# Kernel tuning notes

Measured on AMD Instinct MI355X. Metric: run time of the kernel, lower is better.

## Reference

```python
import jax, jax.numpy as jnp
import numpy as np
from jax import lax

WIN = 9
PAD = WIN // 2
DIM = 3
WIN_VOL = WIN ** DIM  # 729
EPS_DENOM = 1e-05


def _box_sum(x):
    # x: (N, 1, D, H, W); all-ones WINxWINxWIN box filter, 'same' padding
    kernel = jnp.ones((1, 1, WIN, WIN, WIN), dtype=x.dtype)
    return lax.conv_general_dilated(
        x, kernel,
        window_strides=(1, 1, 1),
        padding=[(PAD, PAD)] * 3,
        dimension_numbers=("NCDHW", "OIDHW", "NCDHW"),
    )


def setup_inputs() -> dict:
    key = jax.random.key(0)
    k1, k2 = jax.random.split(key)
    shape = (2, 1, 160, 192, 160)
    I = jax.random.uniform(k1, shape, dtype=jnp.float32)
    J = jax.random.uniform(k2, shape, dtype=jnp.float32)
    return {"I": I, "J": J}


def reference(I, J):
    n = I.shape[0]
    # Fuse the five box-filter convs into one by stacking along the batch dim
    stacked = jnp.concatenate([I, J, I * I, J * J, I * J], axis=0)
    sums = _box_sum(stacked)
    I_sum, J_sum, I2_sum, J2_sum, IJ_sum = (
        sums[0 * n:1 * n], sums[1 * n:2 * n], sums[2 * n:3 * n],
        sums[3 * n:4 * n], sums[4 * n:5 * n],
    )
    wv = jnp.asarray(WIN_VOL, dtype=I.dtype)
    E_I = I_sum / wv
    E_J = J_sum / wv
    cross = IJ_sum - I_sum * E_J - J_sum * E_I + E_I * E_J * wv
    I_var = I2_sum - 2 * E_I * I_sum + E_I * E_I * wv
    J_var = J2_sum - 2 * E_J * J_sum + E_J * E_J * wv
    cc = cross * cross / (I_var * J_var + EPS_DENOM)
    return -jnp.mean(cc)
```

## Files before the change

kernel.cpp:

```cpp
#include <hip/hip_runtime.h>


namespace {
constexpr int Wd = 160, Hd = 192, Dd = 160, NB = 2;
constexpr long DSTRIDE = (long)Hd * Wd;
constexpr long VOLUME  = (long)Dd * DSTRIDE;
constexpr long TOTAL   = VOLUME * NB;
constexpr int BW = 32, BH = 16, BD = 28;
constexpr int EH = BH + 8;
constexpr int NWB = 5, NHB = 12, NDB = 6;
constexpr int NBLK = NB * NDB * NHB * NWB;
constexpr int NT = 512;
constexpr int CH  = EH * BW;
constexpr int HWC = BH * BW;
constexpr float INV_WV = 1.0f / 729.0f;
}

__device__ __forceinline__ void bar_lds() {
    asm volatile("s_waitcnt lgkmcnt(0)\n\ts_barrier" ::: "memory");
}

__device__ __forceinline__ float4 slide9(float v0, float v1, float v2, float v3,
                                         float v4, float v5, float v6, float v7,
                                         float v8, float v9, float v10, float v11) {
    float s8 = ((v0 + v1) + (v2 + v3)) + ((v4 + v5) + (v6 + v7)) + v8;
    float4 o;
    o.x = s8;
    o.y = o.x + (v9 - v0);
    o.z = o.y + (v10 - v1);
    o.w = o.z + (v11 - v2);
    return o;
}

__global__ __launch_bounds__(NT) void k_ncc(const float* __restrict__ I,
                                            const float* __restrict__ J,
                                            float* __restrict__ partial) {
    __shared__ float ws[5 * CH];
    __shared__ float hw[5 * HWC];
    __shared__ float red[NT];

    const int tid = threadIdx.x;
    int bx = blockIdx.x;
    const int wb = bx % NWB; bx /= NWB;
    const int hb = bx % NHB; bx /= NHB;
    const int db = bx % NDB; bx /= NDB;
    const int n  = bx;
    const int w0 = wb * BW, h0 = hb * BH, d0 = db * BD;
    const long nvol = (long)n * VOLUME;

    const int seg = tid & 7;
    const int yy  = tid >> 3;
    const bool aJob = (tid < 192);
    const int ah    = h0 - 4 + yy;
    const int wbase = w0 - 4 + (seg << 2);
    const bool ahOk = aJob && ((unsigned)ah < (unsigned)Hd);
    const bool qok0 = ((unsigned)(wbase + 0) < (unsigned)Wd);
    const bool qok1 = ((unsigned)(wbase + 4) < (unsigned)Wd);
    const bool qok2 = ((unsigned)(wbase + 8) < (unsigned)Wd);
    const long roff = nvol + (long)ah * Wd + wbase + (long)(d0 - 4) * DSTRIDE;
    const float* aI = I + roff;
    const float* aJ = J + roff;

    const int c2  = tid >> 6;
    const int ho0 = ((tid >> 5) & 1) * 8;
    const int w2  = tid & 31;

    const int tx = tid & 31, ty = tid >> 5;

    float4 pI0, pI1, pI2, pJ0, pJ1, pJ2;

#define ISSUE(PP)                                                            \
    do {                                                                     \
        const bool _pv = ahOk && ((unsigned)(PP) < (unsigned)Dd);            \
        pI0 = (_pv && qok0) ? *(const float4*)(aI + 0) : float4{0, 0, 0, 0}; \
        pI1 = (_pv && qok1) ? *(const float4*)(aI + 4) : float4{0, 0, 0, 0}; \
        pI2 = (_pv && qok2) ? *(const float4*)(aI + 8) : float4{0, 0, 0, 0}; \
        pJ0 = (_pv && qok0) ? *(const float4*)(aJ + 0) : float4{0, 0, 0, 0}; \
        pJ1 = (_pv && qok1) ? *(const float4*)(aJ + 4) : float4{0, 0, 0, 0}; \
        pJ2 = (_pv && qok2) ? *(const float4*)(aJ + 8) : float4{0, 0, 0, 0}; \
    } while (0)

    float hist[9][5];
#pragma unroll
    for (int k = 0; k < 9; ++k)
#pragma unroll
        for (int c = 0; c < 5; ++c) hist[k][c] = 0.0f;
    float sa[5] = {0, 0, 0, 0, 0};
    float acc = 0.0f;

    ISSUE(d0 - 4);

#pragma unroll 1
    for (int M = 0; M < 4; ++M) {
#pragma unroll
        for (int u = 0; u < 9; ++u) {
            const int t = 9 * M + u;
            const int p = d0 - 4 + t;
            const bool pvalid = ((unsigned)p < (unsigned)Dd);

            if (pvalid && aJob) {
                const float a0 = pI0.x, a1 = pI0.y, a2 = pI0.z, a3 = pI0.w;
                const float a4 = pI1.x, a5 = pI1.y, a6 = pI1.z, a7 = pI1.w;
                const float a8 = pI2.x, a9 = pI2.y, a10 = pI2.z, a11 = pI2.w;
                const float b0 = pJ0.x, b1 = pJ0.y, b2 = pJ0.z, b3 = pJ0.w;
                const float b4 = pJ1.x, b5 = pJ1.y, b6 = pJ1.z, b7 = pJ1.w;
                const float b8 = pJ2.x, b9 = pJ2.y, b10 = pJ2.z, b11 = pJ2.w;
                float* const wab = ws + yy * BW + (seg << 2);
                *(float4*)(wab + 0 * CH) =
                    slide9(a0, a1, a2, a3, a4, a5, a6, a7, a8, a9, a10, a11);
                *(float4*)(wab + 1 * CH) =
                    slide9(b0, b1, b2, b3, b4, b5, b6, b7, b8, b9, b10, b11);
                *(float4*)(wab + 2 * CH) =
                    slide9(a0 * a0, a1 * a1, a2 * a2, a3 * a3, a4 * a4, a5 * a5,
                           a6 * a6, a7 * a7, a8 * a8, a9 * a9, a10 * a10, a11 * a11);
                *(float4*)(wab + 3 * CH) =
                    slide9(b0 * b0, b1 * b1, b2 * b2, b3 * b3, b4 * b4, b5 * b5,
                           b6 * b6, b7 * b7, b8 * b8, b9 * b9, b10 * b10, b11 * b11);
                *(float4*)(wab + 4 * CH) =
                    slide9(a0 * b0, a1 * b1, a2 * b2, a3 * b3, a4 * b4, a5 * b5,
                           a6 * b6, a7 * b7, a8 * b8, a9 * b9, a10 * b10, a11 * b11);
            }
            aI += DSTRIDE; aJ += DSTRIDE;
            ISSUE(p + 1);

            bar_lds();

            if (pvalid && tid < 320) {
                const float* const src = ws + c2 * CH + ho0 * BW + w2;
                float* const dst = hw + c2 * HWC + ho0 * BW + w2;
                float s = ((src[0 * BW] + src[1 * BW]) + (src[2 * BW] + src[3 * BW]))
                        + ((src[4 * BW] + src[5 * BW]) + (src[6 * BW] + src[7 * BW]));
#pragma unroll
                for (int k = 0; k < 8; ++k) {
                    s += src[(k + 8) * BW];
                    dst[k * BW] = s;
                    s -= src[k * BW];
                }
            }

            bar_lds();

            float h5[5];
            if (pvalid) {
#pragma unroll
                for (int c = 0; c < 5; ++c)
                    h5[c] = hw[c * HWC + ty * BW + tx];
            } else {
#pragma unroll
                for (int c = 0; c < 5; ++c) h5[c] = 0.0f;
            }
#pragma unroll
            for (int c = 0; c < 5; ++c) sa[c] += h5[c];
            const int dout = d0 + t - 8;
            if (t >= 8 && dout < Dd) {
                const float cross = sa[4] - sa[0] * sa[1] * INV_WV;
                const float iv    = sa[2] - sa[0] * sa[0] * INV_WV;
                const float jv    = sa[3] - sa[1] * sa[1] * INV_WV;
                acc += (cross * cross) * __builtin_amdgcn_rcpf(iv * jv + 1e-5f);
            }
#pragma unroll
            for (int c = 0; c < 5; ++c) sa[c] -= hist[(u + 1) % 9][c];
#pragma unroll
            for (int c = 0; c < 5; ++c) hist[u][c] = h5[c];
        }
    }
#undef ISSUE

    red[tid] = acc;
    __syncthreads();
    for (int off = NT / 2; off > 0; off >>= 1) {
        if (tid < off) red[tid] += red[tid + off];
        __syncthreads();
    }
    if (tid == 0) partial[blockIdx.x] = red[0];
}

__global__ __launch_bounds__(256) void k_final(const float* __restrict__ partial,
                                               float* __restrict__ out, int nparts) {
    __shared__ double red[256];
    double a = 0.0;
    for (int i = threadIdx.x; i < nparts; i += 256) a += (double)partial[i];
    red[threadIdx.x] = a;
    __syncthreads();
    for (int off = 128; off > 0; off >>= 1) {
        if (threadIdx.x < off) red[threadIdx.x] += red[threadIdx.x + off];
        __syncthreads();
    }
    if (threadIdx.x == 0) out[0] = (float)(-red[0] / (double)TOTAL);
}

extern "C" void kernel_launch(void* const* d_in, const int* in_sizes, int n_in,
                              void* d_out, int out_size, void* d_ws, size_t ws_size,
                              hipStream_t stream) {
    const float* I = (const float*)d_in[0];
    const float* J = (const float*)d_in[1];
    float* partial = (float*)d_ws;
    float* out = (float*)d_out;

    k_ncc<<<NBLK, NT, 0, stream>>>(I, J, partial);
    k_final<<<1, 256, 0, stream>>>(partial, out, NBLK);
}
```

Measured before the change: 161.5 us.

## Software-pipeline LDS stages with double buffers and one barrier per slice

Double-buffers the two shared-memory staging arrays so stage A (W-direction sums) for slice p+2, stage A2 (H-direction sums) for slice p+1 and the D-direction accumulation for slice p all run in the same iteration. This cuts the barriers per depth slice from two to one. The final reduction kernel is replaced by a memset plus per-block float atomicAdd of scaled partials. The cost is double the LDS footprint, which may limit occupancy, and a float atomic sum whose result is nondeterministic and less precise than the previous double-precision reduction.

```diff
diff --git a/kernel.cpp b/kernel.cpp
--- a/kernel.cpp
+++ b/kernel.cpp
@@ -14,6 +14,7 @@
 constexpr int CH  = EH * BW;
 constexpr int HWC = BH * BW;
 constexpr float INV_WV = 1.0f / 729.0f;
+constexpr float NEG_INV_TOTAL = -1.0f / 9830400.0f;
 }
 
 __device__ __forceinline__ void bar_lds() {
@@ -34,9 +35,9 @@
 
 __global__ __launch_bounds__(NT) void k_ncc(const float* __restrict__ I,
                                             const float* __restrict__ J,
-                                            float* __restrict__ partial) {
-    __shared__ float ws[5 * CH];
-    __shared__ float hw[5 * HWC];
+                                            float* __restrict__ out) {
+    __shared__ float ws[2][5 * CH];
+    __shared__ float hw[2][5 * HWC];
     __shared__ float red[NT];
 
     const int tid = threadIdx.x;
@@ -80,6 +81,44 @@
         pJ2 = (_pv && qok2) ? *(const float4*)(aJ + 8) : float4{0, 0, 0, 0}; \
     } while (0)
 
+#define STAGE_A(WSP, PV)                                                       \
+    if ((PV) && aJob) {                                                        \
+        const float a0 = pI0.x, a1 = pI0.y, a2 = pI0.z, a3 = pI0.w;            \
+        const float a4 = pI1.x, a5 = pI1.y, a6 = pI1.z, a7 = pI1.w;            \
+        const float a8 = pI2.x, a9 = pI2.y, a10 = pI2.z, a11 = pI2.w;          \
+        const float b0 = pJ0.x, b1 = pJ0.y, b2 = pJ0.z, b3 = pJ0.w;            \
+        const float b4 = pJ1.x, b5 = pJ1.y, b6 = pJ1.z, b7 = pJ1.w;            \
+        const float b8 = pJ2.x, b9 = pJ2.y, b10 = pJ2.z, b11 = pJ2.w;          \
+        float* const wab = (WSP) + yy * BW + (seg << 2);                       \
+        *(float4*)(wab + 0 * CH) =                                             \
+            slide9(a0, a1, a2, a3, a4, a5, a6, a7, a8, a9, a10, a11);          \
+        *(float4*)(wab + 1 * CH) =                                             \
+            slide9(b0, b1, b2, b3, b4, b5, b6, b7, b8, b9, b10, b11);          \
+        *(float4*)(wab + 2 * CH) =                                             \
+            slide9(a0 * a0, a1 * a1, a2 * a2, a3 * a3, a4 * a4, a5 * a5,       \
+                   a6 * a6, a7 * a7, a8 * a8, a9 * a9, a10 * a10, a11 * a11);  \
+        *(float4*)(wab + 3 * CH) =                                             \
+            slide9(b0 * b0, b1 * b1, b2 * b2, b3 * b3, b4 * b4, b5 * b5,       \
+                   b6 * b6, b7 * b7, b8 * b8, b9 * b9, b10 * b10, b11 * b11);  \
+        *(float4*)(wab + 4 * CH) =                                             \
+            slide9(a0 * b0, a1 * b1, a2 * b2, a3 * b3, a4 * b4, a5 * b5,       \
+                   a6 * b6, a7 * b7, a8 * b8, a9 * b9, a10 * b10, a11 * b11);  \
+    }
+
+#define STAGE_A2(WSR, HWW, PV)                                                 \
+    if ((PV) && tid < 320) {                                                   \
+        const float* const src = (WSR) + c2 * CH + ho0 * BW + w2;              \
+        float* const dst = (HWW) + c2 * HWC + ho0 * BW + w2;                   \
+        float s = ((src[0 * BW] + src[1 * BW]) + (src[2 * BW] + src[3 * BW]))  \
+                + ((src[4 * BW] + src[5 * BW]) + (src[6 * BW] + src[7 * BW])); \
+        _Pragma("unroll")                                                      \
+        for (int k = 0; k < 8; ++k) {                                          \
+            s += src[(k + 8) * BW];                                            \
+            dst[k * BW] = s;                                                   \
+            s -= src[k * BW];                                                  \
+        }                                                                      \
+    }
+
     float hist[9][5];
 #pragma unroll
     for (int k = 0; k < 9; ++k)
@@ -90,61 +129,45 @@
 
     ISSUE(d0 - 4);
 
+    {
+        const int pA = d0 - 4;
+        STAGE_A(ws[0], (unsigned)pA < (unsigned)Dd);
+        aI += DSTRIDE; aJ += DSTRIDE;
+        ISSUE(pA + 1);
+        bar_lds();
+    }
+    {
+        const int pA = d0 - 3;
+        STAGE_A(ws[1], (unsigned)pA < (unsigned)Dd);
+        aI += DSTRIDE; aJ += DSTRIDE;
+        ISSUE(pA + 1);
+        STAGE_A2(ws[0], hw[0], (unsigned)(d0 - 4) < (unsigned)Dd);
+        bar_lds();
+    }
+
 #pragma unroll 1
     for (int M = 0; M < 4; ++M) {
+        const int mpar = M & 1;
 #pragma unroll
         for (int u = 0; u < 9; ++u) {
-            const int t = 9 * M + u;
-            const int p = d0 - 4 + t;
-            const bool pvalid = ((unsigned)p < (unsigned)Dd);
-
-            if (pvalid && aJob) {
-                const float a0 = pI0.x, a1 = pI0.y, a2 = pI0.z, a3 = pI0.w;
-                const float a4 = pI1.x, a5 = pI1.y, a6 = pI1.z, a7 = pI1.w;
-                const float a8 = pI2.x, a9 = pI2.y, a10 = pI2.z, a11 = pI2.w;
-                const float b0 = pJ0.x, b1 = pJ0.y, b2 = pJ0.z, b3 = pJ0.w;
-                const float b4 = pJ1.x, b5 = pJ1.y, b6 = pJ1.z, b7 = pJ1.w;
-                const float b8 = pJ2.x, b9 = pJ2.y, b10 = pJ2.z, b11 = pJ2.w;
-                float* const wab = ws + yy * BW + (seg << 2);
-                *(float4*)(wab + 0 * CH) =
-                    slide9(a0, a1, a2, a3, a4, a5, a6, a7, a8, a9, a10, a11);
-                *(float4*)(wab + 1 * CH) =
-                    slide9(b0, b1, b2, b3, b4, b5, b6, b7, b8, b9, b10, b11);
-                *(float4*)(wab + 2 * CH) =
-                    slide9(a0 * a0, a1 * a1, a2 * a2, a3 * a3, a4 * a4, a5 * a5,
-                           a6 * a6, a7 * a7, a8 * a8, a9 * a9, a10 * a10, a11 * a11);
-                *(float4*)(wab + 3 * CH) =
-                    slide9(b0 * b0, b1 * b1, b2 * b2, b3 * b3, b4 * b4, b5 * b5,
-                           b6 * b6, b7 * b7, b8 * b8, b9 * b9, b10 * b10, b11 * b11);
-                *(float4*)(wab + 4 * CH) =
-                    slide9(a0 * b0, a1 * b1, a2 * b2, a3 * b3, a4 * b4, a5 * b5,
-                           a6 * b6, a7 * b7, a8 * b8, a9 * b9, a10 * b10, a11 * b11);
-            }
+            const int t   = 9 * M + u;
+            const int pB  = d0 - 4 + t;
+            const int pA2 = pB + 1;
+            const int pA  = pB + 2;
+            const int parA  = (mpar + u) & 1;
+            const int parA2 = (mpar + u + 1) & 1;
+
+            STAGE_A(ws[parA], (t <= 33) && ((unsigned)pA < (unsigned)Dd));
             aI += DSTRIDE; aJ += DSTRIDE;
-            ISSUE(p + 1);
-
-            bar_lds();
-
-            if (pvalid && tid < 320) {
-                const float* const src = ws + c2 * CH + ho0 * BW + w2;
-                float* const dst = hw + c2 * HWC + ho0 * BW + w2;
-                float s = ((src[0 * BW] + src[1 * BW]) + (src[2 * BW] + src[3 * BW]))
-                        + ((src[4 * BW] + src[5 * BW]) + (src[6 * BW] + src[7 * BW]));
-#pragma unroll
-                for (int k = 0; k < 8; ++k) {
-                    s += src[(k + 8) * BW];
-                    dst[k * BW] = s;
-                    s -= src[k * BW];
-                }
-            }
-
-            bar_lds();
+            if (M < 3 || u <= 5) { ISSUE(pA + 1); }
+
+            STAGE_A2(ws[parA2], hw[parA2], (t <= 34) && ((unsigned)pA2 < (unsigned)Dd));
 
             float h5[5];
-            if (pvalid) {
-#pragma unroll
-                for (int c = 0; c < 5; ++c)
-                    h5[c] = hw[c * HWC + ty * BW + tx];
+            if ((unsigned)pB < (unsigned)Dd) {
+                const float* const hb5 = hw[parA] + ty * BW + tx;
+#pragma unroll
+                for (int c = 0; c < 5; ++c) h5[c] = hb5[c * HWC];
             } else {
 #pragma unroll
                 for (int c = 0; c < 5; ++c) h5[c] = 0.0f;
@@ -162,9 +185,13 @@
             for (int c = 0; c < 5; ++c) sa[c] -= hist[(u + 1) % 9][c];
 #pragma unroll
             for (int c = 0; c < 5; ++c) hist[u][c] = h5[c];
+
+            bar_lds();
         }
     }
 #undef ISSUE
+#undef STAGE_A
+#undef STAGE_A2
 
     red[tid] = acc;
     __syncthreads();
@@ -172,21 +199,7 @@
         if (tid < off) red[tid] += red[tid + off];
         __syncthreads();
     }
-    if (tid == 0) partial[blockIdx.x] = red[0];
-}
-
-__global__ __launch_bounds__(256) void k_final(const float* __restrict__ partial,
-                                               float* __restrict__ out, int nparts) {
-    __shared__ double red[256];
-    double a = 0.0;
-    for (int i = threadIdx.x; i < nparts; i += 256) a += (double)partial[i];
-    red[threadIdx.x] = a;
-    __syncthreads();
-    for (int off = 128; off > 0; off >>= 1) {
-        if (threadIdx.x < off) red[threadIdx.x] += red[threadIdx.x + off];
-        __syncthreads();
-    }
-    if (threadIdx.x == 0) out[0] = (float)(-red[0] / (double)TOTAL);
+    if (tid == 0) atomicAdd(out, red[0] * NEG_INV_TOTAL);
 }
 
 extern "C" void kernel_launch(void* const* d_in, const int* in_sizes, int n_in,
@@ -194,9 +207,8 @@
                               hipStream_t stream) {
     const float* I = (const float*)d_in[0];
     const float* J = (const float*)d_in[1];
-    float* partial = (float*)d_ws;
     float* out = (float*)d_out;
 
-    k_ncc<<<NBLK, NT, 0, stream>>>(I, J, partial);
-    k_final<<<1, 256, 0, stream>>>(partial, out, NBLK);
-}
+    hipMemsetAsync(d_out, 0, sizeof(float), stream);
+    k_ncc<<<NBLK, NT, 0, stream>>>(I, J, out);
+}
```

Result: no change. 161.4 us (-0.1%).
